# Kernel tuning notes

Measured on AMD Instinct MI355X. Metric: run time of the kernel, lower is better.

Reference implementation:

```python
import jax, jax.numpy as jnp
import numpy as np

S = 32          # input grid resolution
N = 2048        # active input voxels
C = 256         # in channels
CO = 128        # out channels
S2 = 2 * S      # upsampled resolution
M = 8 * N       # candidate child voxels
EPS = 1e-6


def setup_inputs() -> dict:
    key = jax.random.key(0)
    ks = jax.random.split(key, 8)
    # unique voxel coordinates (sparse occupancy)
    lin = jax.random.permutation(ks[0], S ** 3)[:N]
    coords = jnp.stack([lin // (S * S), (lin // S) % S, lin % S], axis=-1).astype(jnp.int32)
    sc = 0.05
    return {
        "feats": jax.random.normal(ks[1], (N, C), jnp.float32),
        "norm1_w": 1.0 + 0.1 * jax.random.normal(ks[2], (C,), jnp.float32),
        "norm1_b": 0.1 * jax.random.normal(ks[3], (C,), jnp.float32),
        "subdiv_w": sc * jax.random.normal(ks[4], (C, 8), jnp.float32),
        "subdiv_b": jnp.zeros((8,), jnp.float32),
        "conv1_w": sc * jax.random.normal(ks[5], (27, C, CO), jnp.float32),
        "conv1_b": jnp.zeros((CO,), jnp.float32),
        "conv2_w": sc * jax.random.normal(ks[6], (27, CO, CO), jnp.float32),
        "conv2_b": jnp.zeros((CO,), jnp.float32),
        "skip_w": sc * jax.random.normal(ks[7], (C, CO), jnp.float32),
        "skip_b": jnp.zeros((CO,), jnp.float32),
        "coords": coords,
    }


def _layernorm(x, w=None, b=None):
    # LayerNorm32: fp32 math, eps=1e-6
    m = jnp.mean(x, axis=-1, keepdims=True)
    v = jnp.var(x, axis=-1, keepdims=True)
    y = (x - m) * jax.lax.rsqrt(v + EPS)
    if w is not None:
        y = y * w + b
    return y


def _sparse_conv(feats, nidx, w, b):
    # submanifold 3x3x3 sparse conv: gather 27 neighbors, contract.
    # nidx: [M,27] with sentinel M pointing at a zero row.
    pad = jnp.concatenate([feats, jnp.zeros((1, feats.shape[1]), feats.dtype)], axis=0)
    g = pad[nidx]                                   # [M, 27, Cin]
    return jnp.einsum('nkc,kcd->nd', g, w) + b


def _forward(feats, norm1_w, norm1_b, subdiv_w, subdiv_b, conv1_w, conv1_b,
             conv2_w, conv2_b, skip_w, skip_b, coords):
    # subdiv prediction (SparseLinear C -> 8)
    subdiv = feats @ subdiv_w + subdiv_b            # [N, 8]
    # norm1 + silu
    h = jax.nn.silu(_layernorm(feats, norm1_w, norm1_b))
    # sparse upsample x2 with octree subdivision mask
    mask = (subdiv > 0).reshape(-1)                 # [M]
    j = jnp.arange(8, dtype=jnp.int32)
    offs8 = jnp.stack([(j >> 2) & 1, (j >> 1) & 1, j & 1], axis=-1)  # [8,3]
    cc = (coords[:, None, :] * 2 + offs8[None]).reshape(-1, 3)        # [M,3]
    h_c = jnp.where(mask[:, None], jnp.repeat(h, 8, axis=0), 0.0)     # [M,C]
    x_c = jnp.where(mask[:, None], jnp.repeat(feats, 8, axis=0), 0.0)
    # neighbor lookup grid (padded by 1; default M -> zero feature row)
    grid = jnp.full((S2 + 2, S2 + 2, S2 + 2), M, jnp.int32)
    grid = grid.at[cc[:, 0] + 1, cc[:, 1] + 1, cc[:, 2] + 1].set(
        jnp.arange(M, dtype=jnp.int32))
    d = jnp.arange(-1, 2, dtype=jnp.int32)
    offs27 = jnp.stack(jnp.meshgrid(d, d, d, indexing='ij'), axis=-1).reshape(27, 3)
    nc = cc[:, None, :] + 1 + offs27[None]          # [M,27,3]
    nidx = grid[nc[..., 0], nc[..., 1], nc[..., 2]] # [M,27]
    # conv1 -> norm2 (no affine) -> silu -> conv2
    h1 = jax.nn.silu(_layernorm(_sparse_conv(h_c, nidx, conv1_w, conv1_b)))
    h2 = _sparse_conv(h1, nidx, conv2_w, conv2_b)
    # residual with linear skip; mask out non-subdivided children
    out = (h2 + x_c @ skip_w + skip_b) * mask[:, None].astype(h2.dtype)
    return out, subdiv


def reference(feats, norm1_w, norm1_b, subdiv_w, subdiv_b, conv1_w, conv1_b,
              conv2_w, conv2_b, skip_w, skip_b, coords):
    return _forward(feats, norm1_w, norm1_b, subdiv_w, subdiv_b, conv1_w,
                    conv1_b, conv2_w, conv2_b, skip_w, skip_b, coords)
```

## Files before the change

kernel.cpp:

```cpp
#include <hip/hip_runtime.h>
#include <cstdint>
#include <cstddef>

constexpr int N  = 2048;
constexpr int C  = 256;
constexpr int CO = 128;
constexpr int M  = 16384;
constexpr int G  = 66;
constexpr int KP = 7;
constexpr int KCHUNK = 4;
constexpr float EPS = 1e-6f;

using bf8 = __attribute__((ext_vector_type(8))) short;
using f4  = __attribute__((ext_vector_type(4))) float;

static __device__ __forceinline__ unsigned short f2bf(float f) {
  unsigned u = __float_as_uint(f);
  u += 0x7fffu + ((u >> 16) & 1u);
  return (unsigned short)(u >> 16);
}
static __device__ __forceinline__ float bf2f(unsigned short s) {
  return __uint_as_float((unsigned)s << 16);
}

__global__ void k_prep(int* __restrict__ grid, unsigned short* __restrict__ h,
                       unsigned short* __restrict__ h1,
                       const float* __restrict__ c1w, unsigned short* __restrict__ w1t,
                       const float* __restrict__ c2w, unsigned short* __restrict__ w2t) {
  int i = blockIdx.x * 256 + threadIdx.x;
  if (i < G * G * G) grid[i] = M;
  if (i < C)  h[(size_t)N * C + i] = 0;
  if (i < CO) h1[(size_t)M * CO + i] = 0;
  if (i < 27 * C * CO) {
    int c = i % C;
    int rest = i / C;
    int o = rest % CO;
    int k = rest / CO;
    w1t[i] = f2bf(c1w[((size_t)(k * C + c)) * CO + o]);
  }
  if (i < 27 * CO * CO) {
    int c = i % CO;
    int rest = i / CO;
    int o = rest % CO;
    int k = rest / CO;
    w2t[i] = f2bf(c2w[((size_t)(k * CO + c)) * CO + o]);
  }
}

__global__ __launch_bounds__(256) void k_rownorm(
    const float* __restrict__ feats, const float* __restrict__ n1w,
    const float* __restrict__ n1b, const float* __restrict__ sdw,
    const float* __restrict__ sdb, float* __restrict__ out_subdiv,
    unsigned short* __restrict__ h, int* __restrict__ pidx,
    float* __restrict__ maskf, const int* __restrict__ coords,
    int* __restrict__ grid) {
  int n = blockIdx.x, t = threadIdx.x;
  float x = feats[(size_t)n * C + t];
  float4 w0 = *(const float4*)(sdw + t * 8);
  float4 w1 = *(const float4*)(sdw + t * 8 + 4);
  float v[10] = {x * w0.x, x * w0.y, x * w0.z, x * w0.w,
                 x * w1.x, x * w1.y, x * w1.z, x * w1.w, x, x * x};
#pragma unroll
  for (int mk = 1; mk < 64; mk <<= 1) {
#pragma unroll
    for (int j = 0; j < 10; ++j) v[j] += __shfl_xor(v[j], mk, 64);
  }
  __shared__ float red[4][10];
  int wave = t >> 6, lane = t & 63;
  if (lane == 0) {
#pragma unroll
    for (int j = 0; j < 10; ++j) red[wave][j] = v[j];
  }
  __syncthreads();
  float sums[10];
#pragma unroll
  for (int j = 0; j < 10; ++j)
    sums[j] = red[0][j] + red[1][j] + red[2][j] + red[3][j];
  float mean = sums[8] / (float)C;
  float var  = sums[9] / (float)C - mean * mean;
  float rstd = rsqrtf(var + EPS);
  if (t < 8) {
    float sd = sums[t] + sdb[t];
    out_subdiv[(size_t)n * 8 + t] = sd;
    bool mk = sd > 0.f;
    pidx[n * 8 + t]  = mk ? n : N;
    maskf[n * 8 + t] = mk ? 1.f : 0.f;
    int xx = coords[n * 3 + 0] * 2 + ((t >> 2) & 1) + 1;
    int yy = coords[n * 3 + 1] * 2 + ((t >> 1) & 1) + 1;
    int zz = coords[n * 3 + 2] * 2 + (t & 1) + 1;
    grid[(xx * G + yy) * G + zz] = n * 8 + t;
  }
  float y  = (x - mean) * rstd * n1w[t] + n1b[t];
  float sl = y / (1.f + __expf(-y));
  h[(size_t)n * C + t] = f2bf(sl);
}

__global__ void k_nidx(const int* __restrict__ coords, const int* __restrict__ grid,
                       const int* __restrict__ pidx, int* __restrict__ nidxt,
                       int* __restrict__ g1t) {
  int idx = blockIdx.x * 256 + threadIdx.x;
  if (idx >= M * 27) return;
  int m = idx & (M - 1);
  int k = idx >> 14;
  int p = m >> 3, j = m & 7;
  int dx = k / 9 - 1;
  int dy = (k / 3) % 3 - 1;
  int dz = k % 3 - 1;
  int x = coords[p * 3 + 0] * 2 + ((j >> 2) & 1) + 1 + dx;
  int y = coords[p * 3 + 1] * 2 + ((j >> 1) & 1) + 1 + dy;
  int z = coords[p * 3 + 2] * 2 + (j & 1) + 1 + dz;
  int gv = grid[(x * G + y) * G + z];
  nidxt[idx] = gv;
  g1t[idx] = (gv == M) ? N : pidx[gv];
}

__global__ __launch_bounds__(256) void k_skip(const float* __restrict__ feats,
                                              const float* __restrict__ skw,
                                              const float* __restrict__ skb,
                                              float* __restrict__ s) {
  __shared__ float tile[32][36];
  int t = threadIdx.x;
  int rb = (blockIdx.x >> 1) * 32;
  int ob = (blockIdx.x & 1) * 64;
  int o = ob + (t & 63);
  int rg = (t >> 6) * 8;
  float acc[8] = {0, 0, 0, 0, 0, 0, 0, 0};
  for (int cb = 0; cb < C; cb += 32) {
    __syncthreads();
    int row = t >> 3, cc = (t & 7) * 4;
    *(float4*)&tile[row][cc] =
        *(const float4*)(feats + (size_t)(rb + row) * C + cb + cc);
    __syncthreads();
    for (int c = 0; c < 32; ++c) {
      float wv = skw[(size_t)(cb + c) * CO + o];
#pragma unroll
      for (int r = 0; r < 8; ++r) acc[r] += tile[rg + r][c] * wv;
    }
  }
  float bv = skb[o];
#pragma unroll
  for (int r = 0; r < 8; ++r) s[(size_t)(rb + rg + r) * CO + o] = acc[r] + bv;
}

template <int CIN, int NCB>
__global__ __launch_bounds__(256, 3) void k_conv(
    const unsigned short* __restrict__ src, const int* __restrict__ gt,
    const unsigned short* __restrict__ wt, unsigned short* __restrict__ part) {
  __shared__ unsigned short sA[2][128 * 32];
  __shared__ unsigned short sB[2][128 * 32];
  const int t = threadIdx.x;
  const int w = t >> 6, lane = t & 63;
  const int quad = lane >> 4, ln = lane & 15;
  const int m0 = blockIdx.x * 128;
  const int kpart = blockIdx.y;
  const int k0 = kpart * KCHUNK;
  const int nk = min(KCHUNK, 27 - k0);
  const int nstage = nk * NCB;
  const int rh = (w >> 1) * 64, ch = (w & 1) * 64;

  const int row2 = t >> 1;
  const int c0 = (t & 1) * 2;
  const int x3 = (row2 >> 1) & 3;
  const int wsl0 = row2 * 32 + ((c0) ^ x3) * 8;
  const int wsl1 = row2 * 32 + ((c0 + 1) ^ x3) * 8;

  int ga[KCHUNK];
#pragma unroll
  for (int kk = 0; kk < KCHUNK; ++kk)
    ga[kk] = (kk < nk) ? gt[(size_t)(k0 + kk) * M + m0 + row2] : 0;

  bf8 ra0, ra1, rb0, rb1;
  auto loadreg = [&](int s) {
    const int kk = s / NCB;
    const int cb = s - kk * NCB;
    const unsigned short* pa = src + (size_t)ga[kk] * CIN + cb * 32 + c0 * 8;
    const unsigned short* pb =
        wt + ((size_t)(k0 + kk) * CO + row2) * CIN + cb * 32 + c0 * 8;
    ra0 = *(const bf8*)(pa);
    ra1 = *(const bf8*)(pa + 8);
    rb0 = *(const bf8*)(pb);
    rb1 = *(const bf8*)(pb + 8);
  };
  auto writelds = [&](int buf) {
    *(bf8*)(sA[buf] + wsl0) = ra0;
    *(bf8*)(sA[buf] + wsl1) = ra1;
    *(bf8*)(sB[buf] + wsl0) = rb0;
    *(bf8*)(sB[buf] + wsl1) = rb1;
  };

  f4 acc[16];
  f4 zero = {0.f, 0.f, 0.f, 0.f};
#pragma unroll
  for (int i = 0; i < 16; ++i) acc[i] = zero;

  const int slot = (quad ^ ((ln >> 1) & 3)) * 8;

  loadreg(0);
  writelds(0);
  for (int s = 0; s < nstage; ++s) {
    const bool have = (s + 1 < nstage);
    if (have) loadreg(s + 1);
    __syncthreads();
    const unsigned short* pa = sA[s & 1];
    const unsigned short* pb = sB[s & 1];
    bf8 av[4], bv[4];
#pragma unroll
    for (int ti = 0; ti < 4; ++ti)
      av[ti] = *(const bf8*)(pa + (rh + ti * 16 + ln) * 32 + slot);
#pragma unroll
    for (int tj = 0; tj < 4; ++tj)
      bv[tj] = *(const bf8*)(pb + (ch + tj * 16 + ln) * 32 + slot);
#pragma unroll
    for (int ti = 0; ti < 4; ++ti)
#pragma unroll
      for (int tj = 0; tj < 4; ++tj)
        acc[ti * 4 + tj] = __builtin_amdgcn_mfma_f32_16x16x32_bf16(
            av[ti], bv[tj], acc[ti * 4 + tj], 0, 0, 0);
    if (have) writelds((s + 1) & 1);
  }

  unsigned short* pp = part + ((size_t)kpart * M + m0) * CO;
#pragma unroll
  for (int ti = 0; ti < 4; ++ti) {
    int mrow = rh + ti * 16 + quad * 4;
#pragma unroll
    for (int tj = 0; tj < 4; ++tj) {
      int co = ch + tj * 16 + ln;
#pragma unroll
      for (int rr = 0; rr < 4; ++rr)
        pp[(size_t)(mrow + rr) * CO + co] = f2bf(acc[ti * 4 + tj][rr]);
    }
  }
}

__global__ __launch_bounds__(256) void k_r1(const unsigned short* __restrict__ p,
                                            const float* __restrict__ bias,
                                            unsigned short* __restrict__ h1) {
  int wave = threadIdx.x >> 6, lane = threadIdx.x & 63;
  int m = blockIdx.x * 4 + wave;
  float v0 = bias[lane], v1 = bias[lane + 64];
#pragma unroll
  for (int q = 0; q < KP; ++q) {
    const unsigned short* pq = p + ((size_t)q * M + m) * CO;
    v0 += bf2f(pq[lane]);
    v1 += bf2f(pq[lane + 64]);
  }
  float sum = v0 + v1, sq = v0 * v0 + v1 * v1;
#pragma unroll
  for (int mk = 1; mk < 64; mk <<= 1) {
    sum += __shfl_xor(sum, mk, 64);
    sq  += __shfl_xor(sq, mk, 64);
  }
  float mean = sum / (float)CO;
  float var  = sq / (float)CO - mean * mean;
  float rstd = rsqrtf(var + EPS);
  float y0 = (v0 - mean) * rstd;
  float y1 = (v1 - mean) * rstd;
  float s0 = y0 / (1.f + __expf(-y0));
  float s1 = y1 / (1.f + __expf(-y1));
  h1[(size_t)m * CO + lane]      = f2bf(s0);
  h1[(size_t)m * CO + lane + 64] = f2bf(s1);
}

__global__ __launch_bounds__(256) void k_r2(const unsigned short* __restrict__ p,
                                            const float* __restrict__ bias,
                                            const float* __restrict__ sres,
                                            const float* __restrict__ maskf,
                                            float* __restrict__ out) {
  int i = blockIdx.x * 256 + threadIdx.x;
  int m = i >> 5;
  int o4 = (i & 31) * 4;
  float4 acc = *(const float4*)(bias + o4);
#pragma unroll
  for (int q = 0; q < KP; ++q) {
    ushort4 a = *(const ushort4*)(p + ((size_t)q * M + m) * CO + o4);
    acc.x += bf2f(a.x); acc.y += bf2f(a.y);
    acc.z += bf2f(a.z); acc.w += bf2f(a.w);
  }
  float4 s = *(const float4*)(sres + (size_t)(m >> 3) * CO + o4);
  float mk = maskf[m];
  float4 r;
  r.x = (acc.x + s.x) * mk;
  r.y = (acc.y + s.y) * mk;
  r.z = (acc.z + s.z) * mk;
  r.w = (acc.w + s.w) * mk;
  *(float4*)(out + (size_t)m * CO + o4) = r;
}

extern "C" void kernel_launch(void* const* d_in, const int* in_sizes, int n_in,
                              void* d_out, int out_size, void* d_ws, size_t ws_size,
                              hipStream_t stream) {
  const float* feats = (const float*)d_in[0];
  const float* n1w   = (const float*)d_in[1];
  const float* n1b   = (const float*)d_in[2];
  const float* sdw   = (const float*)d_in[3];
  const float* sdb   = (const float*)d_in[4];
  const float* c1w   = (const float*)d_in[5];
  const float* c1b   = (const float*)d_in[6];
  const float* c2w   = (const float*)d_in[7];
  const float* c2b   = (const float*)d_in[8];
  const float* skw   = (const float*)d_in[9];
  const float* skb   = (const float*)d_in[10];
  const int* coords  = (const int*)d_in[11];
  float* out = (float*)d_out;

  char* ws = (char*)d_ws;
  size_t off = 0;
  auto alloc = [&](size_t bytes) -> char* {
    char* p = ws + off;
    off += (bytes + 255) & ~(size_t)255;
    return p;
  };
  unsigned short* h    = (unsigned short*)alloc((size_t)(N + 1) * C * 2);
  unsigned short* h1   = (unsigned short*)alloc((size_t)(M + 1) * CO * 2);
  int*   grid  = (int*)alloc((size_t)G * G * G * 4);
  int*   nidxt = (int*)alloc((size_t)27 * M * 4);
  int*   g1t   = (int*)alloc((size_t)27 * M * 4);
  int*   pidx  = (int*)alloc((size_t)M * 4);
  float* maskf = (float*)alloc((size_t)M * 4);
  float* sres  = (float*)alloc((size_t)N * CO * 4);
  unsigned short* w1t = (unsigned short*)alloc((size_t)27 * CO * C * 2);
  unsigned short* w2t = (unsigned short*)alloc((size_t)27 * CO * CO * 2);
  unsigned short* pc  = (unsigned short*)alloc((size_t)KP * M * CO * 2);

  k_prep<<<(27 * C * CO + 255) / 256, 256, 0, stream>>>(grid, h, h1, c1w, w1t,
                                                        c2w, w2t);
  k_rownorm<<<N, 256, 0, stream>>>(feats, n1w, n1b, sdw, sdb,
                                   out + (size_t)M * CO, h, pidx, maskf,
                                   coords, grid);
  k_nidx<<<(M * 27 + 255) / 256, 256, 0, stream>>>(coords, grid, pidx, nidxt, g1t);
  k_skip<<<128, 256, 0, stream>>>(feats, skw, skb, sres);

  k_conv<C, 8><<<dim3(M / 128, KP), 256, 0, stream>>>(h, g1t, w1t, pc);
  k_r1<<<M / 4, 256, 0, stream>>>(pc, c1b, h1);

  k_conv<CO, 4><<<dim3(M / 128, KP), 256, 0, stream>>>(h1, nidxt, w2t, pc);
  k_r2<<<M * CO / 4 / 256, 256, 0, stream>>>(pc, c2b, sres, maskf, out);
}
```

Baseline: 190.6 us.

## Gather conv A operands straight into registers and coalesce weight transpose

The sparse-conv kernel no longer stages the gathered activation tile through LDS. Each lane loads its MFMA A fragment directly from global memory using the neighbor indices, and prefetches the next stage into registers. Only the weight tile stays double-buffered in shared memory. The weight transpose in the prep kernel now uses a 32x32 shared-memory tile so that both its reads and writes are coalesced. The K split changes from 7 chunks of 4 offsets to 4 chunks of 7, which shrinks the partial-sum buffer that the reduction kernels must read. The trade-offs are narrower 16-byte scattered global loads, higher register pressure (launch bounds lowered to 2 blocks per SM), and fewer blocks in the conv grid.

```diff
diff --git a/kernel.cpp b/kernel.cpp
--- a/kernel.cpp
+++ b/kernel.cpp
@@ -7,8 +7,8 @@
 constexpr int CO = 128;
 constexpr int M  = 16384;
 constexpr int G  = 66;
-constexpr int KP = 7;
-constexpr int KCHUNK = 4;
+constexpr int KP = 4;
+constexpr int KCHUNK = 7;
 constexpr float EPS = 1e-6f;
 
 using bf8 = __attribute__((ext_vector_type(8))) short;
@@ -23,27 +23,43 @@
   return __uint_as_float((unsigned)s << 16);
 }
 
-__global__ void k_prep(int* __restrict__ grid, unsigned short* __restrict__ h,
-                       unsigned short* __restrict__ h1,
-                       const float* __restrict__ c1w, unsigned short* __restrict__ w1t,
-                       const float* __restrict__ c2w, unsigned short* __restrict__ w2t) {
+__global__ __launch_bounds__(256) void k_prep(
+    const float* __restrict__ c1w, unsigned short* __restrict__ w1t,
+    const float* __restrict__ c2w, unsigned short* __restrict__ w2t,
+    int* __restrict__ grid, unsigned short* __restrict__ h,
+    unsigned short* __restrict__ h1) {
   int i = blockIdx.x * 256 + threadIdx.x;
   if (i < G * G * G) grid[i] = M;
-  if (i < C)  h[(size_t)N * C + i] = 0;
-  if (i < CO) h1[(size_t)M * CO + i] = 0;
-  if (i < 27 * C * CO) {
-    int c = i % C;
-    int rest = i / C;
-    int o = rest % CO;
-    int k = rest / CO;
-    w1t[i] = f2bf(c1w[((size_t)(k * C + c)) * CO + o]);
-  }
-  if (i < 27 * CO * CO) {
-    int c = i % CO;
-    int rest = i / CO;
-    int o = rest % CO;
-    int k = rest / CO;
-    w2t[i] = f2bf(c2w[((size_t)(k * CO + c)) * CO + o]);
+  if (blockIdx.x == 1200) {
+    if (threadIdx.x < C) h[(size_t)N * C + threadIdx.x] = 0;
+  }
+  if (blockIdx.x == 1201) {
+    if (threadIdx.x < CO) h1[(size_t)M * CO + threadIdx.x] = 0;
+  }
+
+  __shared__ float tile[32][33];
+  int bx = blockIdx.x;
+  const float* w; unsigned short* wtp; int cin, k, cb, ob;
+  if (bx < 864) {
+    w = c1w; wtp = w1t; cin = C;
+    k = bx >> 5; int tl = bx & 31; cb = tl >> 2; ob = tl & 3;
+  } else {
+    int b2 = bx - 864;
+    w = c2w; wtp = w2t; cin = CO;
+    k = b2 >> 4; int tl = b2 & 15; cb = tl >> 2; ob = tl & 3;
+  }
+  int ty = threadIdx.x >> 5, tx = threadIdx.x & 31;
+#pragma unroll
+  for (int j = 0; j < 4; ++j) {
+    int row = ty + j * 8;
+    tile[row][tx] = w[((size_t)k * cin + cb * 32 + row) * CO + ob * 32 + tx];
+  }
+  __syncthreads();
+#pragma unroll
+  for (int j = 0; j < 4; ++j) {
+    int row = ty + j * 8;
+    wtp[((size_t)k * CO + ob * 32 + row) * cin + cb * 32 + tx] =
+        f2bf(tile[tx][row]);
   }
 }
 
@@ -143,10 +159,9 @@
 }
 
 template <int CIN, int NCB>
-__global__ __launch_bounds__(256, 3) void k_conv(
+__global__ __launch_bounds__(256, 2) void k_conv(
     const unsigned short* __restrict__ src, const int* __restrict__ gt,
     const unsigned short* __restrict__ wt, unsigned short* __restrict__ part) {
-  __shared__ unsigned short sA[2][128 * 32];
   __shared__ unsigned short sB[2][128 * 32];
   const int t = threadIdx.x;
   const int w = t >> 6, lane = t & 63;
@@ -163,27 +178,22 @@
   const int x3 = (row2 >> 1) & 3;
   const int wsl0 = row2 * 32 + ((c0) ^ x3) * 8;
   const int wsl1 = row2 * 32 + ((c0 + 1) ^ x3) * 8;
-
-  int ga[KCHUNK];
-#pragma unroll
-  for (int kk = 0; kk < KCHUNK; ++kk)
-    ga[kk] = (kk < nk) ? gt[(size_t)(k0 + kk) * M + m0 + row2] : 0;
-
-  bf8 ra0, ra1, rb0, rb1;
-  auto loadreg = [&](int s) {
-    const int kk = s / NCB;
-    const int cb = s - kk * NCB;
-    const unsigned short* pa = src + (size_t)ga[kk] * CIN + cb * 32 + c0 * 8;
+  const int slot = (quad ^ ((ln >> 1) & 3)) * 8;
+
+  const int* gbase = gt + (size_t)k0 * M + m0 + rh + ln;
+
+  bf8 rb0, rb1;
+  bf8 ra[4], rn[4];
+  int ga[4], gn[4];
+
+  auto loadB = [&](int s) {
+    const int kk = s / NCB, cb = s - kk * NCB;
     const unsigned short* pb =
         wt + ((size_t)(k0 + kk) * CO + row2) * CIN + cb * 32 + c0 * 8;
-    ra0 = *(const bf8*)(pa);
-    ra1 = *(const bf8*)(pa + 8);
     rb0 = *(const bf8*)(pb);
     rb1 = *(const bf8*)(pb + 8);
   };
-  auto writelds = [&](int buf) {
-    *(bf8*)(sA[buf] + wsl0) = ra0;
-    *(bf8*)(sA[buf] + wsl1) = ra1;
+  auto writeB = [&](int buf) {
     *(bf8*)(sB[buf] + wsl0) = rb0;
     *(bf8*)(sB[buf] + wsl1) = rb1;
   };
@@ -193,20 +203,33 @@
 #pragma unroll
   for (int i = 0; i < 16; ++i) acc[i] = zero;
 
-  const int slot = (quad ^ ((ln >> 1) & 3)) * 8;
-
-  loadreg(0);
-  writelds(0);
+#pragma unroll
+  for (int ti = 0; ti < 4; ++ti) ga[ti] = gbase[ti * 16];
+  loadB(0);
+#pragma unroll
+  for (int ti = 0; ti < 4; ++ti)
+    ra[ti] = *(const bf8*)(src + (size_t)ga[ti] * CIN + quad * 8);
+  writeB(0);
+
   for (int s = 0; s < nstage; ++s) {
+    const int buf = s & 1;
+    const int kk = s / NCB, cb = s - kk * NCB;
     const bool have = (s + 1 < nstage);
-    if (have) loadreg(s + 1);
+    if (cb == 0 && kk + 1 < nk) {
+#pragma unroll
+      for (int ti = 0; ti < 4; ++ti) gn[ti] = gbase[(size_t)(kk + 1) * M + ti * 16];
+    }
+    if (have) {
+      loadB(s + 1);
+      const int cb1 = (cb + 1 < NCB) ? cb + 1 : 0;
+      const int* gu = (cb + 1 < NCB) ? ga : gn;
+#pragma unroll
+      for (int ti = 0; ti < 4; ++ti)
+        rn[ti] = *(const bf8*)(src + (size_t)gu[ti] * CIN + cb1 * 32 + quad * 8);
+    }
     __syncthreads();
-    const unsigned short* pa = sA[s & 1];
-    const unsigned short* pb = sB[s & 1];
-    bf8 av[4], bv[4];
-#pragma unroll
-    for (int ti = 0; ti < 4; ++ti)
-      av[ti] = *(const bf8*)(pa + (rh + ti * 16 + ln) * 32 + slot);
+    const unsigned short* pb = sB[buf];
+    bf8 bv[4];
 #pragma unroll
     for (int tj = 0; tj < 4; ++tj)
       bv[tj] = *(const bf8*)(pb + (ch + tj * 16 + ln) * 32 + slot);
@@ -215,8 +238,16 @@
 #pragma unroll
       for (int tj = 0; tj < 4; ++tj)
         acc[ti * 4 + tj] = __builtin_amdgcn_mfma_f32_16x16x32_bf16(
-            av[ti], bv[tj], acc[ti * 4 + tj], 0, 0, 0);
-    if (have) writelds((s + 1) & 1);
+            ra[ti], bv[tj], acc[ti * 4 + tj], 0, 0, 0);
+    if (have) {
+      writeB(buf ^ 1);
+#pragma unroll
+      for (int ti = 0; ti < 4; ++ti) ra[ti] = rn[ti];
+      if (cb + 1 == NCB) {
+#pragma unroll
+        for (int ti = 0; ti < 4; ++ti) ga[ti] = gn[ti];
+      }
+    }
   }
 
   unsigned short* pp = part + ((size_t)kpart * M + m0) * CO;
@@ -323,8 +354,7 @@
   unsigned short* w2t = (unsigned short*)alloc((size_t)27 * CO * CO * 2);
   unsigned short* pc  = (unsigned short*)alloc((size_t)KP * M * CO * 2);
 
-  k_prep<<<(27 * C * CO + 255) / 256, 256, 0, stream>>>(grid, h, h1, c1w, w1t,
-                                                        c2w, w2t);
+  k_prep<<<1296, 256, 0, stream>>>(c1w, w1t, c2w, w2t, grid, h, h1);
   k_rownorm<<<N, 256, 0, stream>>>(feats, n1w, n1b, sdw, sdb,
                                    out + (size_t)M * CO, h, pidx, maskf,
                                    coords, grid);
```

New measurement: 198.4 us. +4.1%, slower.
